# Performance work log

Measured on AMD Instinct MI355X. Metric: run time of the kernel, lower is better.

The kernel has to match this reference:

```python
import jax, jax.numpy as jnp
import numpy as np


def log_g(x):
    # log of g(x) = x + 0.5 if x >= 0 else sigmoid(x)  (minGRU paper Appendix B)
    return jnp.where(x >= 0, jnp.log(jax.nn.relu(x) + 0.5), -jax.nn.softplus(-x))


def parallel_scan_log(log_coeffs, log_values):
    # log_coeffs: [B, T, H]; log_values: [B, T+1, H]
    a_star = jnp.pad(jnp.cumsum(log_coeffs, axis=1), ((0, 0), (1, 0), (0, 0)))  # [B, T+1, H]
    log_h = a_star + jax.lax.cumlogsumexp(log_values - a_star, axis=1)
    return jnp.exp(log_h)  # [B, T+1, H]


def setup_inputs() -> dict:
    key = jax.random.key(0)
    ks = jax.random.split(key, 6)
    B, T, D, H = 4, 4096, 1024, 1024
    scale = 1.0 / np.sqrt(D)
    return {
        "x": jax.random.normal(ks[0], (B, T, D), dtype=jnp.float32),
        "h_0": jax.random.uniform(ks[1], (B, H), dtype=jnp.float32),
        "Wz": jax.random.normal(ks[2], (H, D), dtype=jnp.float32) * scale,
        "bz": jnp.zeros((H,), dtype=jnp.float32),
        "Wh": jax.random.normal(ks[3], (H, D), dtype=jnp.float32) * scale,
        "bh": jnp.zeros((H,), dtype=jnp.float32),
    }


def reference(x, h_0, Wz, bz, Wh, bh):
    T = x.shape[1]
    k = jnp.einsum("btd,hd->bth", x, Wz) + bz          # linear_z(x)
    log_z = -jax.nn.softplus(-k)                          # log sigmoid(k)
    log_coeffs = -jax.nn.softplus(k)                      # log (1 - sigmoid(k))
    log_h_0 = log_g(h_0)[:, None, :]                      # [B, 1, H]
    log_tilde_h = log_g(jnp.einsum("btd,hd->bth", x, Wh) + bh)
    log_values = jnp.concatenate([log_h_0, log_z + log_tilde_h], axis=1)  # [B, T+1, H]
    h = parallel_scan_log(log_coeffs, log_values)
    return h[:, -T:, :]
```

## Files before the change

### kernel.cpp

```cpp
#include <hip/hip_runtime.h>
#include <hip/hip_bf16.h>
#include <hip/hip_fp16.h>

#define B_ 4
#define T_ 4096
#define D_ 1024
#define H_ 1024
#define M_ (B_ * T_)

typedef __attribute__((ext_vector_type(8))) short short8;
typedef __attribute__((ext_vector_type(4))) float f32x4;

__device__ __forceinline__ unsigned short f2bf(float f) {
    unsigned int u = __float_as_uint(f);
    u += 0x7fffu + ((u >> 16) & 1u);
    return (unsigned short)(u >> 16);
}

__global__ __launch_bounds__(256) void convert_all(
    const float* __restrict__ x, const float* __restrict__ wz, const float* __restrict__ wh,
    unsigned short* __restrict__ xbp, unsigned short* __restrict__ wcbp)
{
    int i = blockIdx.x * 256 + threadIdx.x;
    const float* srcrow;
    unsigned short* dst;
    if (i < 2097152) {
        int l = i & 63, s = i >> 6;
        int c = s & 31, r = s >> 5;
        int row = r * 16 + (l & 15);
        int k   = c * 32 + (l >> 4) * 8;
        srcrow = x + (size_t)row * D_ + k;
        dst = xbp + (size_t)i * 8;
    } else {
        int j = i - 2097152;
        int l = j & 63, s = j >> 6;
        int c = s & 31, r = s >> 5;
        int ir = r * 16 + (l & 15);
        int a = ir >> 5, wi = ir & 31;
        const float* m = (wi < 16) ? wz : wh;
        int srow = a * 16 + (wi & 15);
        int k = c * 32 + (l >> 4) * 8;
        srcrow = m + (size_t)srow * D_ + k;
        dst = wcbp + (size_t)j * 8;
    }
    float4 f0 = ((const float4*)srcrow)[0];
    float4 f1 = ((const float4*)srcrow)[1];
    ushort4 u0, u1;
    u0.x = f2bf(f0.x); u0.y = f2bf(f0.y); u0.z = f2bf(f0.z); u0.w = f2bf(f0.w);
    u1.x = f2bf(f1.x); u1.y = f2bf(f1.y); u1.z = f2bf(f1.z); u1.w = f2bf(f1.w);
    ((ushort4*)dst)[0] = u0;
    ((ushort4*)dst)[1] = u1;
}

__device__ __forceinline__ void async16(const void* g, void* l) {
    __builtin_amdgcn_global_load_lds(
        (__attribute__((address_space(1))) void*)g,
        (__attribute__((address_space(3))) void*)l,
        16, 0, 0);
}

#define BARRIER() do { asm volatile("" ::: "memory"); __builtin_amdgcn_s_barrier(); asm volatile("" ::: "memory"); } while (0)
#define VMW(n)    asm volatile("s_waitcnt vmcnt(" #n ")" ::: "memory")

__global__ __launch_bounds__(512, 2) void dual_gemm_kernel(
    const unsigned short* __restrict__ xbp,
    const unsigned short* __restrict__ wcbp,
    const float* __restrict__ bz,
    const float* __restrict__ bh,
    __half2* __restrict__ av16,
    float2* __restrict__ chunkAV)
{
    __shared__ short8 ldsA[2 * 2 * 16 * 64];

    const int tid  = threadIdx.x;
    const int lane = tid & 63;
    const int w    = __builtin_amdgcn_readfirstlane(tid >> 6);
    const int wr   = w >> 2;
    const int wc   = w & 3;
    const int r16  = lane & 15;
    const int q    = lane >> 4;

    const int bid = blockIdx.x;
    const int swz = (bid & 7) * 64 + (bid >> 3);
    const int nb  = swz & 7;
    const int mb  = swz >> 3;

    const unsigned short* gAp = xbp + ((size_t)mb * 16 * 32) * 512 + lane * 8;
    const unsigned short* gBd = wcbp + ((size_t)(nb * 16 + wc * 4) * 32) * 512 + lane * 8;

#define STAGE_A(tt, pp) do { \
    _Pragma("unroll") \
    for (int kh = 0; kh < 2; ++kh) { \
        _Pragma("unroll") \
        for (int d = 0; d < 2; ++d) { \
            const unsigned short* _s = gAp + (size_t)(((2 * w + d) * 32 + (tt) * 2 + kh)) * 512; \
            short8* _dst = &ldsA[(pp) * 2048 + kh * 1024 + (2 * w + d) * 64]; \
            async16(_s, _dst); \
        } } } while (0)

#define LOADB(DST, tt) do { \
    _Pragma("unroll") \
    for (int n = 0; n < 4; ++n) { \
        _Pragma("unroll") \
        for (int kh = 0; kh < 2; ++kh) { \
            DST[n][kh] = *(const short8*)(gBd + (size_t)((n * 32 + (tt) * 2 + kh)) * 512); \
        } } } while (0)

    f32x4 acc[8][4] = {};
    short8 fbA[4][2], fbB[4][2];

    STAGE_A(0, 0);
    LOADB(fbA, 0);

#define GROUP(g, CUR, NXT) do { \
    const int _p = (g) & 1; \
    if ((g) < 15) { STAGE_A((g) + 1, _p ^ 1); LOADB(NXT, (g) + 1); VMW(12); } \
    else          { VMW(0); } \
    BARRIER(); \
    const int _oA = _p * 2048 + wr * 512; \
    { \
        short8 fa0[4], fa1[4]; \
        _Pragma("unroll") \
        for (int m = 0; m < 4; ++m) fa0[m] = ldsA[_oA + m * 64 + lane]; \
        _Pragma("unroll") \
        for (int m = 0; m < 4; ++m) fa1[m] = ldsA[_oA + (4 + m) * 64 + lane]; \
        __builtin_amdgcn_s_setprio(1); \
        _Pragma("unroll") \
        for (int m = 0; m < 4; ++m) \
            _Pragma("unroll") \
            for (int n = 0; n < 4; ++n) \
                acc[m][n] = __builtin_amdgcn_mfma_f32_16x16x32_bf16(fa0[m], CUR[n][0], acc[m][n], 0, 0, 0); \
        _Pragma("unroll") \
        for (int m = 0; m < 4; ++m) \
            _Pragma("unroll") \
            for (int n = 0; n < 4; ++n) \
                acc[4 + m][n] = __builtin_amdgcn_mfma_f32_16x16x32_bf16(fa1[m], CUR[n][0], acc[4 + m][n], 0, 0, 0); \
        __builtin_amdgcn_s_setprio(0); \
    } \
    { \
        short8 fa2[4], fa3[4]; \
        _Pragma("unroll") \
        for (int m = 0; m < 4; ++m) fa2[m] = ldsA[_oA + 1024 + m * 64 + lane]; \
        _Pragma("unroll") \
        for (int m = 0; m < 4; ++m) fa3[m] = ldsA[_oA + 1024 + (4 + m) * 64 + lane]; \
        __builtin_amdgcn_s_setprio(1); \
        _Pragma("unroll") \
        for (int m = 0; m < 4; ++m) \
            _Pragma("unroll") \
            for (int n = 0; n < 4; ++n) \
                acc[m][n] = __builtin_amdgcn_mfma_f32_16x16x32_bf16(fa2[m], CUR[n][1], acc[m][n], 0, 0, 0); \
        _Pragma("unroll") \
        for (int m = 0; m < 4; ++m) \
            _Pragma("unroll") \
            for (int n = 0; n < 4; ++n) \
                acc[4 + m][n] = __builtin_amdgcn_mfma_f32_16x16x32_bf16(fa3[m], CUR[n][1], acc[4 + m][n], 0, 0, 0); \
        __builtin_amdgcn_s_setprio(0); \
    } \
    BARRIER(); \
} while (0)

    for (int it = 0; it < 8; ++it) {
        GROUP(2 * it,     fbA, fbB);
        GROUP(2 * it + 1, fbB, fbA);
    }

    const int mrow0 = mb * 256 + wr * 128;
#pragma unroll
    for (int gg = 0; gg < 2; ++gg) {
        const int ncol = nb * 128 + wc * 32 + gg * 16 + r16;
        const float bzv = bz[ncol];
        const float bhv = bh[ncol];
#pragma unroll
        for (int hh = 0; hh < 2; ++hh) {
            float CA = 1.0f, CV = 0.0f;
#pragma unroll
            for (int mm = 0; mm < 4; ++mm) {
                const int mf = hh * 4 + mm;
                float LA = 1.0f, LV = 0.0f;
#pragma unroll
                for (int rr = 0; rr < 4; ++rr) {
                    float kv = acc[mf][2 * gg + 0][rr] + bzv;
                    float hv = acc[mf][2 * gg + 1][rr] + bhv;
                    float tk = __expf(-fabsf(kv));
                    float ik = 1.0f / (1.0f + tk);
                    float sig = (kv >= 0.0f) ? ik : tk * ik;
                    float ac  = (kv >= 0.0f) ? tk * ik : ik;
                    float th = __expf(-fabsf(hv));
                    float ih = 1.0f / (1.0f + th);
                    float gh = (hv >= 0.0f) ? (hv + 0.5f) : th * ih;
                    float vv = sig * gh;
                    const size_t m = (size_t)(mrow0 + mf * 16 + q * 4 + rr);
                    av16[m * H_ + ncol] = __floats2half2_rn(ac, vv);
                    LV = ac * LV + vv;
                    LA = ac * LA;
                }
#pragma unroll
                for (int mask = 16; mask <= 32; mask <<= 1) {
                    float PA = __shfl_xor(LA, mask);
                    float PV = __shfl_xor(LV, mask);
                    if (lane & mask) { LV = LA * PV + LV; LA = LA * PA; }
                    else             { LV = PA * LV + PV; LA = PA * LA; }
                }
                CV = LA * CV + LV;
                CA = LA * CA;
            }
            if (q == 0) {
                const int cglob = mb * 4 + wr * 2 + hh;
                chunkAV[(cglob & 63) * 4096 + (cglob >> 6) * 1024 + ncol] = make_float2(CA, CV);
            }
        }
    }
#undef STAGE_A
#undef LOADB
#undef GROUP
}

__global__ __launch_bounds__(256) void scan_pass2(const float2* __restrict__ chunkAV,
                                                  const float* __restrict__ h0,
                                                  float* __restrict__ hstart) {
    int chan = blockIdx.x * blockDim.x + threadIdx.x;
    int n = chan & (H_ - 1);
    int b = chan >> 10;
    float x = h0[b * H_ + n];
    float h;
    if (x >= 0.0f) { h = x + 0.5f; }
    else { float t = __expf(x); h = t / (1.0f + t); }
#pragma unroll 8
    for (int c = 0; c < 64; ++c) {
        hstart[c * 4096 + chan] = h;
        float2 s = chunkAV[c * 4096 + chan];
        h = s.x * h + s.y;
    }
}

__global__ __launch_bounds__(256) void scan_pass3(const __half2* __restrict__ av16,
                                                  const float* __restrict__ hstart,
                                                  float* __restrict__ out) {
    int g = blockIdx.x * blockDim.x + threadIdx.x;
    int n = g & (H_ - 1);
    int rest = g >> 10;
    int c = rest & 63;
    int b = rest >> 6;
    float h = hstart[c * 4096 + b * 1024 + n];
    const __half2* base = av16 + ((size_t)(b * T_ + c * 64)) * H_ + n;
    float* obase = out + ((size_t)(b * T_ + c * 64)) * H_ + n;
#pragma unroll 8
    for (int t = 0; t < 64; ++t) {
        float2 p = __half22float2(base[(size_t)t * H_]);
        h = p.x * h + p.y;
        obase[(size_t)t * H_] = h;
    }
}

extern "C" void kernel_launch(void* const* d_in, const int* in_sizes, int n_in,
                              void* d_out, int out_size, void* d_ws, size_t ws_size,
                              hipStream_t stream) {
    const float* x  = (const float*)d_in[0];
    const float* h0 = (const float*)d_in[1];
    const float* Wz = (const float*)d_in[2];
    const float* bz = (const float*)d_in[3];
    const float* Wh = (const float*)d_in[4];
    const float* bh = (const float*)d_in[5];
    float* out = (float*)d_out;

    char* ws = (char*)d_ws;
    unsigned short* xbp  = (unsigned short*)(ws);
    unsigned short* wcbp = (unsigned short*)(ws + 33554432);
    __half2* av16        = (__half2*)(ws + 37748736);
    float2* chunkAV      = (float2*)(ws + 104857600);
    float*  hstart       = (float*)(ws + 106954752);

    convert_all<<<9216, 256, 0, stream>>>(x, Wz, Wh, xbp, wcbp);

    dual_gemm_kernel<<<512, 512, 0, stream>>>(xbp, wcbp, bz, bh, av16, chunkAV);

    scan_pass2<<<16,   256, 0, stream>>>(chunkAV, h0, hstart);
    scan_pass3<<<1024, 256, 0, stream>>>(av16, hstart, out);
}
```

Before: 242.2 us.

## Replace LDS-staged GEMM with direct register loads and fold carry scan into pass3

The packed bf16 layout is reordered so that K-chunks are outermost. The GEMM drops LDS staging and barriers: each wave loads its A and B fragments straight from global memory into registers with double buffering, and blocks shrink to 256 threads, 1024 of them. The separate chunk-carry scan kernel is removed, and each pass3 thread recomputes its starting state by serially combining the previous chunk summaries. This removes a launch and the LDS synchronisation. In exchange, A fragments are no longer shared across waves through LDS, and pass3 threads do up to 63 extra redundant loads.

```diff
diff --git a/kernel.cpp b/kernel.cpp
--- a/kernel.cpp
+++ b/kernel.cpp
@@ -30,7 +30,7 @@
         int row = r * 16 + (l & 15);
         int k   = c * 32 + (l >> 4) * 8;
         srcrow = x + (size_t)row * D_ + k;
-        dst = xbp + (size_t)i * 8;
+        dst = xbp + ((size_t)(c * 1024 + r) * 64 + l) * 8;
     } else {
         int j = i - 2097152;
         int l = j & 63, s = j >> 6;
@@ -41,7 +41,7 @@
         int srow = a * 16 + (wi & 15);
         int k = c * 32 + (l >> 4) * 8;
         srcrow = m + (size_t)srow * D_ + k;
-        dst = wcbp + (size_t)j * 8;
+        dst = wcbp + ((size_t)(c * 128 + r) * 64 + l) * 8;
     }
     float4 f0 = ((const float4*)srcrow)[0];
     float4 f1 = ((const float4*)srcrow)[1];
@@ -52,17 +52,7 @@
     ((ushort4*)dst)[1] = u1;
 }
 
-__device__ __forceinline__ void async16(const void* g, void* l) {
-    __builtin_amdgcn_global_load_lds(
-        (__attribute__((address_space(1))) void*)g,
-        (__attribute__((address_space(3))) void*)l,
-        16, 0, 0);
-}
-
-#define BARRIER() do { asm volatile("" ::: "memory"); __builtin_amdgcn_s_barrier(); asm volatile("" ::: "memory"); } while (0)
-#define VMW(n)    asm volatile("s_waitcnt vmcnt(" #n ")" ::: "memory")
-
-__global__ __launch_bounds__(512, 2) void dual_gemm_kernel(
+__global__ __launch_bounds__(256, 2) void dual_gemm_kernel(
     const unsigned short* __restrict__ xbp,
     const unsigned short* __restrict__ wcbp,
     const float* __restrict__ bz,
@@ -70,104 +60,55 @@
     __half2* __restrict__ av16,
     float2* __restrict__ chunkAV)
 {
-    __shared__ short8 ldsA[2 * 2 * 16 * 64];
-
     const int tid  = threadIdx.x;
     const int lane = tid & 63;
     const int w    = __builtin_amdgcn_readfirstlane(tid >> 6);
-    const int wr   = w >> 2;
-    const int wc   = w & 3;
     const int r16  = lane & 15;
     const int q    = lane >> 4;
 
     const int bid = blockIdx.x;
-    const int swz = (bid & 7) * 64 + (bid >> 3);
-    const int nb  = swz & 7;
-    const int mb  = swz >> 3;
-
-    const unsigned short* gAp = xbp + ((size_t)mb * 16 * 32) * 512 + lane * 8;
-    const unsigned short* gBd = wcbp + ((size_t)(nb * 16 + wc * 4) * 32) * 512 + lane * 8;
-
-#define STAGE_A(tt, pp) do { \
+    const int swz = (bid & 7) * 128 + (bid >> 3);
+    const int nbg = swz & 7;
+    const int mbw = swz >> 3;
+    const int nbw = nbg * 4 + w;
+
+    const unsigned short* gA = xbp  + (size_t)(mbw * 8) * 512 + lane * 8;
+    const unsigned short* gB = wcbp + (size_t)(nbw * 4) * 512 + lane * 8;
+
+#define LOADK(FA, FB, c) do { \
+    const unsigned short* _a = gA + (size_t)(c) * 524288; \
+    const unsigned short* _b = gB + (size_t)(c) * 65536; \
     _Pragma("unroll") \
-    for (int kh = 0; kh < 2; ++kh) { \
+    for (int m = 0; m < 8; ++m) FA[m] = *(const short8*)(_a + m * 512); \
+    _Pragma("unroll") \
+    for (int n = 0; n < 4; ++n) FB[n] = *(const short8*)(_b + n * 512); \
+} while (0)
+
+#define MFMA32(FA, FB) do { \
+    __builtin_amdgcn_s_setprio(1); \
+    _Pragma("unroll") \
+    for (int m = 0; m < 8; ++m) \
         _Pragma("unroll") \
-        for (int d = 0; d < 2; ++d) { \
-            const unsigned short* _s = gAp + (size_t)(((2 * w + d) * 32 + (tt) * 2 + kh)) * 512; \
-            short8* _dst = &ldsA[(pp) * 2048 + kh * 1024 + (2 * w + d) * 64]; \
-            async16(_s, _dst); \
-        } } } while (0)
-
-#define LOADB(DST, tt) do { \
-    _Pragma("unroll") \
-    for (int n = 0; n < 4; ++n) { \
-        _Pragma("unroll") \
-        for (int kh = 0; kh < 2; ++kh) { \
-            DST[n][kh] = *(const short8*)(gBd + (size_t)((n * 32 + (tt) * 2 + kh)) * 512); \
-        } } } while (0)
+        for (int n = 0; n < 4; ++n) \
+            acc[m][n] = __builtin_amdgcn_mfma_f32_16x16x32_bf16(FA[m], FB[n], acc[m][n], 0, 0, 0); \
+    __builtin_amdgcn_s_setprio(0); \
+} while (0)
 
     f32x4 acc[8][4] = {};
-    short8 fbA[4][2], fbB[4][2];
-
-    STAGE_A(0, 0);
-    LOADB(fbA, 0);
-
-#define GROUP(g, CUR, NXT) do { \
-    const int _p = (g) & 1; \
-    if ((g) < 15) { STAGE_A((g) + 1, _p ^ 1); LOADB(NXT, (g) + 1); VMW(12); } \
-    else          { VMW(0); } \
-    BARRIER(); \
-    const int _oA = _p * 2048 + wr * 512; \
-    { \
-        short8 fa0[4], fa1[4]; \
-        _Pragma("unroll") \
-        for (int m = 0; m < 4; ++m) fa0[m] = ldsA[_oA + m * 64 + lane]; \
-        _Pragma("unroll") \
-        for (int m = 0; m < 4; ++m) fa1[m] = ldsA[_oA + (4 + m) * 64 + lane]; \
-        __builtin_amdgcn_s_setprio(1); \
-        _Pragma("unroll") \
-        for (int m = 0; m < 4; ++m) \
-            _Pragma("unroll") \
-            for (int n = 0; n < 4; ++n) \
-                acc[m][n] = __builtin_amdgcn_mfma_f32_16x16x32_bf16(fa0[m], CUR[n][0], acc[m][n], 0, 0, 0); \
-        _Pragma("unroll") \
-        for (int m = 0; m < 4; ++m) \
-            _Pragma("unroll") \
-            for (int n = 0; n < 4; ++n) \
-                acc[4 + m][n] = __builtin_amdgcn_mfma_f32_16x16x32_bf16(fa1[m], CUR[n][0], acc[4 + m][n], 0, 0, 0); \
-        __builtin_amdgcn_s_setprio(0); \
-    } \
-    { \
-        short8 fa2[4], fa3[4]; \
-        _Pragma("unroll") \
-        for (int m = 0; m < 4; ++m) fa2[m] = ldsA[_oA + 1024 + m * 64 + lane]; \
-        _Pragma("unroll") \
-        for (int m = 0; m < 4; ++m) fa3[m] = ldsA[_oA + 1024 + (4 + m) * 64 + lane]; \
-        __builtin_amdgcn_s_setprio(1); \
-        _Pragma("unroll") \
-        for (int m = 0; m < 4; ++m) \
-            _Pragma("unroll") \
-            for (int n = 0; n < 4; ++n) \
-                acc[m][n] = __builtin_amdgcn_mfma_f32_16x16x32_bf16(fa2[m], CUR[n][1], acc[m][n], 0, 0, 0); \
-        _Pragma("unroll") \
-        for (int m = 0; m < 4; ++m) \
-            _Pragma("unroll") \
-            for (int n = 0; n < 4; ++n) \
-                acc[4 + m][n] = __builtin_amdgcn_mfma_f32_16x16x32_bf16(fa3[m], CUR[n][1], acc[4 + m][n], 0, 0, 0); \
-        __builtin_amdgcn_s_setprio(0); \
-    } \
-    BARRIER(); \
-} while (0)
-
-    for (int it = 0; it < 8; ++it) {
-        GROUP(2 * it,     fbA, fbB);
-        GROUP(2 * it + 1, fbB, fbA);
-    }
-
-    const int mrow0 = mb * 256 + wr * 128;
+    short8 fa0[8], fb0[4], fa1[8], fb1[4];
+
+    LOADK(fa0, fb0, 0);
+    for (int cc = 0; cc < 32; cc += 2) {
+        LOADK(fa1, fb1, cc + 1);
+        MFMA32(fa0, fb0);
+        if (cc < 30) LOADK(fa0, fb0, cc + 2);
+        MFMA32(fa1, fb1);
+    }
+
+    const int mrow0 = mbw * 128;
 #pragma unroll
     for (int gg = 0; gg < 2; ++gg) {
-        const int ncol = nb * 128 + wc * 32 + gg * 16 + r16;
+        const int ncol = nbw * 32 + gg * 16 + r16;
         const float bzv = bz[ncol];
         const float bhv = bh[ncol];
 #pragma unroll
@@ -205,43 +146,32 @@
                 CA = LA * CA;
             }
             if (q == 0) {
-                const int cglob = mb * 4 + wr * 2 + hh;
+                const int cglob = mbw * 2 + hh;
                 chunkAV[(cglob & 63) * 4096 + (cglob >> 6) * 1024 + ncol] = make_float2(CA, CV);
             }
         }
     }
-#undef STAGE_A
-#undef LOADB
-#undef GROUP
-}
-
-__global__ __launch_bounds__(256) void scan_pass2(const float2* __restrict__ chunkAV,
+#undef LOADK
+#undef MFMA32
+}
+
+__global__ __launch_bounds__(256) void scan_pass3(const __half2* __restrict__ av16,
+                                                  const float2* __restrict__ chunkAV,
                                                   const float* __restrict__ h0,
-                                                  float* __restrict__ hstart) {
-    int chan = blockIdx.x * blockDim.x + threadIdx.x;
-    int n = chan & (H_ - 1);
-    int b = chan >> 10;
-    float x = h0[b * H_ + n];
-    float h;
-    if (x >= 0.0f) { h = x + 0.5f; }
-    else { float t = __expf(x); h = t / (1.0f + t); }
-#pragma unroll 8
-    for (int c = 0; c < 64; ++c) {
-        hstart[c * 4096 + chan] = h;
-        float2 s = chunkAV[c * 4096 + chan];
-        h = s.x * h + s.y;
-    }
-}
-
-__global__ __launch_bounds__(256) void scan_pass3(const __half2* __restrict__ av16,
-                                                  const float* __restrict__ hstart,
                                                   float* __restrict__ out) {
     int g = blockIdx.x * blockDim.x + threadIdx.x;
     int n = g & (H_ - 1);
     int rest = g >> 10;
     int c = rest & 63;
     int b = rest >> 6;
-    float h = hstart[c * 4096 + b * 1024 + n];
+    float x = h0[b * H_ + n];
+    float h;
+    if (x >= 0.0f) { h = x + 0.5f; }
+    else { float t = __expf(x); h = t / (1.0f + t); }
+    for (int cc = 0; cc < c; ++cc) {
+        float2 s = chunkAV[cc * 4096 + b * 1024 + n];
+        h = s.x * h + s.y;
+    }
     const __half2* base = av16 + ((size_t)(b * T_ + c * 64)) * H_ + n;
     float* obase = out + ((size_t)(b * T_ + c * 64)) * H_ + n;
 #pragma unroll 8
@@ -268,12 +198,10 @@
     unsigned short* wcbp = (unsigned short*)(ws + 33554432);
     __half2* av16        = (__half2*)(ws + 37748736);
     float2* chunkAV      = (float2*)(ws + 104857600);
-    float*  hstart       = (float*)(ws + 106954752);
 
     convert_all<<<9216, 256, 0, stream>>>(x, Wz, Wh, xbp, wcbp);
 
-    dual_gemm_kernel<<<512, 512, 0, stream>>>(xbp, wcbp, bz, bh, av16, chunkAV);
-
-    scan_pass2<<<16,   256, 0, stream>>>(chunkAV, h0, hstart);
-    scan_pass3<<<1024, 256, 0, stream>>>(av16, hstart, out);
-}
+    dual_gemm_kernel<<<1024, 256, 0, stream>>>(xbp, wcbp, bz, bh, av16, chunkAV);
+
+    scan_pass3<<<1024, 256, 0, stream>>>(av16, chunkAV, h0, out);
+}
```

Measured after the change: 239.6 us. About the same (-1.1%).
